# Optimization experiments

Measured on AMD Instinct MI355X. Metric: run time of the kernel, lower is better.

## Reference

```python
import jax, jax.numpy as jnp
import numpy as np
import math

QUERY_LEN = 64
VALUES_LEN = 64
NUM_HEADS = 16


def setup_inputs() -> dict:
    key = jax.random.key(0)
    k1, k2, k3, k4 = jax.random.split(key, 4)
    B, G, N = 2, 4, 1024
    D = QUERY_LEN * NUM_HEADS  # 1024
    queries = jax.random.normal(k1, (B, G, N, D), dtype=jnp.float32)
    keys = jax.random.normal(k2, (B, G, N, D), dtype=jnp.float32)
    values = jax.random.normal(k3, (B, G, N, VALUES_LEN * NUM_HEADS), dtype=jnp.float32)
    neuron_bank_connectivity_sub = jax.random.uniform(k4, (1, G, 1, N, N), dtype=jnp.float32)
    return {
        "queries": queries,
        "keys": keys,
        "values": values,
        "neuron_bank_connectivity_sub": neuron_bank_connectivity_sub,
    }


def reference(queries, keys, values, neuron_bank_connectivity_sub):
    B, G, N, _ = queries.shape
    H, dq, dv = NUM_HEADS, QUERY_LEN, VALUES_LEN
    # view last dim as (vec_len, num_heads), move heads forward: [B,G,H,N,d]
    q = queries.reshape(B, G, N, dq, H).transpose(0, 1, 4, 2, 3)
    k = keys.reshape(B, G, N, dq, H).transpose(0, 1, 4, 2, 3)
    v = values.reshape(B, G, N, dv, H).transpose(0, 1, 4, 2, 3)
    scores = jnp.einsum('bghnd,bghmd->bghnm', q, k) / math.sqrt(dq)
    probs = jax.nn.softmax(scores - neuron_bank_connectivity_sub, axis=-1)
    out = jnp.einsum('bghnm,bghmd->bghnd', probs, v)  # [B,G,H,N,dv]
    # Faithful to original: view() applied to the contiguous [B,G,H,N,dv] buffer
    return out.reshape(B, G, N, H * dv)
```

## Files before the change

kernel.cpp:

```cpp
#include <hip/hip_runtime.h>
#include <hip/hip_bf16.h>
#include <math.h>

#define B_ 2
#define G_ 4
#define N_ 1024
#define H_ 16
#define D_ 64
#define BG_ (B_*G_)
#define BGH_ (B_*G_*H_)
#define MK 64

typedef __bf16 bf16;
typedef bf16 bf16x8 __attribute__((ext_vector_type(8)));
typedef float f32x4 __attribute__((ext_vector_type(4)));

__global__ __launch_bounds__(256) void transpose_qk(const float* __restrict__ src,
                                                    bf16* __restrict__ dst) {
    int bx   = blockIdx.x;
    int bg   = bx >> 6;
    int tile = bx & 63;
    int t  = threadIdx.x;
    int h  = t & 15;
    int db = (t >> 4) & 7;
    int nh = t >> 7;
    const float* sb = src + (size_t)bg * N_ * 1024;
    bf16* ob = dst + ((size_t)(bg * H_ + h)) * N_ * D_;
#pragma unroll
    for (int np = 0; np < 8; ++np) {
        int n = tile * 16 + np * 2 + nh;
        const float* sr = sb + (size_t)n * 1024 + h;
        bf16x8 v;
#pragma unroll
        for (int k = 0; k < 8; ++k)
            v[k] = (bf16)sr[(db * 8 + k) * 16];
        *(bf16x8*)(ob + (size_t)n * D_ + db * 8) = v;
    }
}

__global__ __launch_bounds__(256) void transpose_v(const float* __restrict__ src,
                                                   bf16* __restrict__ dst) {
    int bx    = blockIdx.x;
    int dq    = bx & 3;
    int ntile = (bx >> 2) & 15;
    int bg    = bx >> 6;
    int t  = threadIdx.x;
    int h  = t & 15;
    int d  = dq * 16 + (t >> 4);
    const float* sb = src + (size_t)bg * N_ * 1024 + d * 16 + h;
    bf16* ob = dst + (((size_t)(bg * H_ + h)) * D_ + d) * N_;
#pragma unroll
    for (int n8 = 0; n8 < 8; ++n8) {
        int n = ntile * 64 + n8 * 8;
        bf16x8 v;
#pragma unroll
        for (int k = 0; k < 8; ++k)
            v[k] = (bf16)sb[(size_t)(n + k) * 1024];
        *(bf16x8*)(ob + n) = v;
    }
}

__global__ __launch_bounds__(256, 4) void flash_kernel(
    const bf16* __restrict__ qt, const bf16* __restrict__ kt, const bf16* __restrict__ vtT,
    const float* __restrict__ bias, float* __restrict__ out)
{
    __shared__ __attribute__((aligned(16))) bf16 k_lds[MK][72];
    __shared__ __attribute__((aligned(16))) bf16 v_lds[D_][72];
    __shared__ __attribute__((aligned(16))) bf16 p_lds[4][16][72];

    int tid  = threadIdx.x;
    int w    = tid >> 6;
    int lane = tid & 63;
    int quad = lane >> 4;
    int col  = lane & 15;

    int bgh = blockIdx.y;
    int n0  = blockIdx.x * 64;
    int g   = (bgh >> 4) & (G_ - 1);

    int qrow = n0 + w * 16 + col;
    const bf16* qbase = qt + ((size_t)bgh * N_ + qrow) * D_;
    bf16x8 aq0 = *(const bf16x8*)(qbase + quad * 8);
    bf16x8 aq1 = *(const bf16x8*)(qbase + 32 + quad * 8);

    f32x4 acc0 = {0,0,0,0}, acc1 = {0,0,0,0}, acc2 = {0,0,0,0}, acc3 = {0,0,0,0};
    float l_part[4] = {0, 0, 0, 0};

    int srow = tid >> 2;
    int soff = (tid & 3) * 16;
    const bf16* kp = kt + (size_t)bgh * N_ * D_ + (size_t)srow * D_ + soff;
    const bf16* vp = vtT + ((size_t)bgh * D_ + srow) * N_ + soff;
    const float* bias_base = bias + (size_t)g * N_ * N_;

    bf16x8 kr0 = *(const bf16x8*)(kp);
    bf16x8 kr1 = *(const bf16x8*)(kp + 8);
    bf16x8 vr0 = *(const bf16x8*)(vp);
    bf16x8 vr1 = *(const bf16x8*)(vp + 8);

    for (int m0 = 0; m0 < N_; m0 += MK) {
        __syncthreads();
        *(bf16x8*)(&k_lds[srow][soff])     = kr0;
        *(bf16x8*)(&k_lds[srow][soff + 8]) = kr1;
        *(bf16x8*)(&v_lds[srow][soff])     = vr0;
        *(bf16x8*)(&v_lds[srow][soff + 8]) = vr1;
        __syncthreads();

        if (m0 + MK < N_) {
            kp += MK * D_;  vp += MK;
            kr0 = *(const bf16x8*)(kp);
            kr1 = *(const bf16x8*)(kp + 8);
            vr0 = *(const bf16x8*)(vp);
            vr1 = *(const bf16x8*)(vp + 8);
        }

        float bl[4][4];
        const float* brow = bias_base + m0 + col;
#pragma unroll
        for (int r = 0; r < 4; ++r) {
            size_t ro = (size_t)(n0 + w * 16 + quad * 4 + r) * N_;
#pragma unroll
            for (int c = 0; c < 4; ++c)
                bl[r][c] = brow[ro + c * 16];
        }

        f32x4 s[4];
        f32x4 z = {0, 0, 0, 0};
#pragma unroll
        for (int c = 0; c < 4; ++c) {
            bf16x8 b0 = *(const bf16x8*)(&k_lds[c * 16 + col][quad * 8]);
            bf16x8 b1 = *(const bf16x8*)(&k_lds[c * 16 + col][32 + quad * 8]);
            s[c] = __builtin_amdgcn_mfma_f32_16x16x32_bf16(aq0, b0, z, 0, 0, 0);
            s[c] = __builtin_amdgcn_mfma_f32_16x16x32_bf16(aq1, b1, s[c], 0, 0, 0);
        }

#pragma unroll
        for (int c = 0; c < 4; ++c) {
#pragma unroll
            for (int r = 0; r < 4; ++r) {
                float p = __expf(s[c][r] * 0.125f - bl[r][c]);
                l_part[r] += p;
                p_lds[w][quad * 4 + r][c * 16 + col] = (bf16)p;
            }
        }

        bf16x8 ap0 = *(const bf16x8*)(&p_lds[w][col][quad * 8]);
        bf16x8 ap1 = *(const bf16x8*)(&p_lds[w][col][32 + quad * 8]);
        {
            bf16x8 bv00 = *(const bf16x8*)(&v_lds[col][quad * 8]);
            bf16x8 bv01 = *(const bf16x8*)(&v_lds[col][32 + quad * 8]);
            acc0 = __builtin_amdgcn_mfma_f32_16x16x32_bf16(ap0, bv00, acc0, 0, 0, 0);
            acc0 = __builtin_amdgcn_mfma_f32_16x16x32_bf16(ap1, bv01, acc0, 0, 0, 0);
            bf16x8 bv10 = *(const bf16x8*)(&v_lds[16 + col][quad * 8]);
            bf16x8 bv11 = *(const bf16x8*)(&v_lds[16 + col][32 + quad * 8]);
            acc1 = __builtin_amdgcn_mfma_f32_16x16x32_bf16(ap0, bv10, acc1, 0, 0, 0);
            acc1 = __builtin_amdgcn_mfma_f32_16x16x32_bf16(ap1, bv11, acc1, 0, 0, 0);
            bf16x8 bv20 = *(const bf16x8*)(&v_lds[32 + col][quad * 8]);
            bf16x8 bv21 = *(const bf16x8*)(&v_lds[32 + col][32 + quad * 8]);
            acc2 = __builtin_amdgcn_mfma_f32_16x16x32_bf16(ap0, bv20, acc2, 0, 0, 0);
            acc2 = __builtin_amdgcn_mfma_f32_16x16x32_bf16(ap1, bv21, acc2, 0, 0, 0);
            bf16x8 bv30 = *(const bf16x8*)(&v_lds[48 + col][quad * 8]);
            bf16x8 bv31 = *(const bf16x8*)(&v_lds[48 + col][32 + quad * 8]);
            acc3 = __builtin_amdgcn_mfma_f32_16x16x32_bf16(ap0, bv30, acc3, 0, 0, 0);
            acc3 = __builtin_amdgcn_mfma_f32_16x16x32_bf16(ap1, bv31, acc3, 0, 0, 0);
        }
    }

#pragma unroll
    for (int r = 0; r < 4; ++r) {
#pragma unroll
        for (int off = 1; off <= 8; off <<= 1)
            l_part[r] += __shfl_xor(l_part[r], off, 64);
    }
#pragma unroll
    for (int r = 0; r < 4; ++r) {
        float inv = 1.0f / l_part[r];
        int rown = n0 + w * 16 + quad * 4 + r;
        float* obase = out + ((size_t)bgh * N_ + rown) * D_ + col;
        obase[0]  = acc0[r] * inv;
        obase[16] = acc1[r] * inv;
        obase[32] = acc2[r] * inv;
        obase[48] = acc3[r] * inv;
    }
}

__global__ __launch_bounds__(256) void naive_kernel(
    const float* __restrict__ q, const float* __restrict__ k,
    const float* __restrict__ v, const float* __restrict__ bias,
    float* __restrict__ out)
{
    __shared__ float sc[N_];
    __shared__ float red[256];
    __shared__ float qrow[64];
    int n = blockIdx.x;
    int bgh = blockIdx.y;
    int bg = bgh >> 4, h = bgh & 15;
    int g = bg & (G_ - 1);
    int tid = threadIdx.x;
    const float* qr = q + ((size_t)(bg * N_ + n)) * 1024;
    if (tid < 64) qrow[tid] = qr[tid * 16 + h];
    __syncthreads();
    const float* bb = bias + (size_t)g * N_ * N_ + (size_t)n * N_;
    for (int m = tid; m < N_; m += 256) {
        const float* kr = k + ((size_t)(bg * N_ + m)) * 1024 + h;
        float dot = 0.f;
        for (int d = 0; d < 64; ++d) dot += qrow[d] * kr[d * 16];
        sc[m] = dot * 0.125f - bb[m];
    }
    __syncthreads();
    float mx = -INFINITY;
    for (int m = tid; m < N_; m += 256) mx = fmaxf(mx, sc[m]);
    red[tid] = mx; __syncthreads();
    for (int s = 128; s > 0; s >>= 1) {
        if (tid < s) red[tid] = fmaxf(red[tid], red[tid + s]);
        __syncthreads();
    }
    float M = red[0]; __syncthreads();
    float sum = 0.f;
    for (int m = tid; m < N_; m += 256) { float e = __expf(sc[m] - M); sc[m] = e; sum += e; }
    red[tid] = sum; __syncthreads();
    for (int s = 128; s > 0; s >>= 1) {
        if (tid < s) red[tid] += red[tid + s];
        __syncthreads();
    }
    float L = red[0]; __syncthreads();
    int d = tid & 63, quarter = tid >> 6;
    float acc = 0.f;
    const float* vb = v + (size_t)bg * N_ * 1024 + d * 16 + h;
    for (int m = quarter * 256; m < quarter * 256 + 256; ++m) acc += sc[m] * vb[(size_t)m * 1024];
    red[tid] = acc; __syncthreads();
    if (tid < 64) {
        float o = (red[tid] + red[tid + 64] + red[tid + 128] + red[tid + 192]) / L;
        out[((size_t)bgh * N_ + n) * 64 + d] = o;
    }
}

extern "C" void kernel_launch(void* const* d_in, const int* in_sizes, int n_in,
                              void* d_out, int out_size, void* d_ws, size_t ws_size,
                              hipStream_t stream) {
    const float* q    = (const float*)d_in[0];
    const float* k    = (const float*)d_in[1];
    const float* v    = (const float*)d_in[2];
    const float* bias = (const float*)d_in[3];
    float* out = (float*)d_out;

    const size_t elems = (size_t)BGH_ * N_ * D_;
    const size_t need  = 3 * elems * sizeof(bf16);

    if (ws_size >= need) {
        bf16* qt  = (bf16*)d_ws;
        bf16* ktb = qt + elems;
        bf16* vtT = ktb + elems;
        transpose_qk<<<BG_ * (N_ / 16), 256, 0, stream>>>(q, qt);
        transpose_qk<<<BG_ * (N_ / 16), 256, 0, stream>>>(k, ktb);
        transpose_v<<<BG_ * 16 * 4, 256, 0, stream>>>(v, vtT);
        dim3 grid(N_ / 64, BGH_);
        flash_kernel<<<grid, 256, 0, stream>>>(qt, ktb, vtT, bias, out);
    } else {
        dim3 grid(N_, BGH_);
        naive_kernel<<<grid, 256, 0, stream>>>(q, k, v, bias, out);
    }
}
```

Before: 234.6 us.

## Fuse QKV transposes via LDS staging and prefetch bias in flash loop

Replaces the three separate strided-gather transpose kernels with one fused kernel. It reads rows with coalesced float4 loads, stages them through LDS, and writes the head-major bf16 layouts, folding the softmax scale and log2e into Q. The flash kernel fully unrolls the key loop and double-buffers the bias loads one tile ahead in registers, and uses exp2 with an fma in place of expf. This targets uncoalesced transpose reads, extra launches and bias load latency, at the cost of more registers and an LDS-heavy transpose with possible bank conflicts on the V path.

```diff
diff --git a/kernel.cpp b/kernel.cpp
--- a/kernel.cpp
+++ b/kernel.cpp
@@ -10,53 +10,71 @@
 #define BG_ (B_*G_)
 #define BGH_ (B_*G_*H_)
 #define MK 64
+#define LOG2E 1.44269504f
+#define QSCALE (0.125f * LOG2E)
 
 typedef __bf16 bf16;
 typedef bf16 bf16x8 __attribute__((ext_vector_type(8)));
 typedef float f32x4 __attribute__((ext_vector_type(4)));
 
-__global__ __launch_bounds__(256) void transpose_qk(const float* __restrict__ src,
-                                                    bf16* __restrict__ dst) {
-    int bx   = blockIdx.x;
-    int bg   = bx >> 6;
-    int tile = bx & 63;
-    int t  = threadIdx.x;
-    int h  = t & 15;
-    int db = (t >> 4) & 7;
-    int nh = t >> 7;
-    const float* sb = src + (size_t)bg * N_ * 1024;
-    bf16* ob = dst + ((size_t)(bg * H_ + h)) * N_ * D_;
-#pragma unroll
-    for (int np = 0; np < 8; ++np) {
-        int n = tile * 16 + np * 2 + nh;
-        const float* sr = sb + (size_t)n * 1024 + h;
-        bf16x8 v;
-#pragma unroll
-        for (int k = 0; k < 8; ++k)
-            v[k] = (bf16)sr[(db * 8 + k) * 16];
-        *(bf16x8*)(ob + (size_t)n * D_ + db * 8) = v;
-    }
-}
-
-__global__ __launch_bounds__(256) void transpose_v(const float* __restrict__ src,
-                                                   bf16* __restrict__ dst) {
-    int bx    = blockIdx.x;
-    int dq    = bx & 3;
-    int ntile = (bx >> 2) & 15;
-    int bg    = bx >> 6;
-    int t  = threadIdx.x;
-    int h  = t & 15;
-    int d  = dq * 16 + (t >> 4);
-    const float* sb = src + (size_t)bg * N_ * 1024 + d * 16 + h;
-    bf16* ob = dst + (((size_t)(bg * H_ + h)) * D_ + d) * N_;
-#pragma unroll
-    for (int n8 = 0; n8 < 8; ++n8) {
-        int n = ntile * 64 + n8 * 8;
-        bf16x8 v;
-#pragma unroll
-        for (int k = 0; k < 8; ++k)
-            v[k] = (bf16)sb[(size_t)(n + k) * 1024];
-        *(bf16x8*)(ob + n) = v;
+#define HS 1160
+#define NS 72
+
+__global__ __launch_bounds__(256) void transpose_fused(
+    const float* __restrict__ q, const float* __restrict__ k, const float* __restrict__ v,
+    bf16* __restrict__ qt, bf16* __restrict__ ktb, bf16* __restrict__ vtT)
+{
+    __shared__ __attribute__((aligned(16))) bf16 lds[16 * HS];
+    int bx = blockIdx.x;
+    int tensor = bx >> 9;
+    int rr = bx & 511;
+    int bg = rr >> 6;
+    int tile = rr & 63;
+    int n0 = tile * 16;
+    int t = threadIdx.x;
+
+    const float* src = (tensor == 0) ? q : (tensor == 1) ? k : v;
+    float scale = (tensor == 0) ? QSCALE : 1.0f;
+    const float* sb = src + (size_t)bg * N_ * 1024 + (size_t)n0 * 1024;
+
+    int h0 = 4 * (t & 3);
+    int d  = t >> 2;
+    int wbase = h0 * HS + d;
+#pragma unroll 4
+    for (int i = 0; i < 16; ++i) {
+        float4 val = ((const float4*)(sb + (size_t)i * 1024))[t];
+        bf16* p = &lds[wbase + i * NS];
+        p[0]        = (bf16)(val.x * scale);
+        p[HS]       = (bf16)(val.y * scale);
+        p[2 * HS]   = (bf16)(val.z * scale);
+        p[3 * HS]   = (bf16)(val.w * scale);
+    }
+    __syncthreads();
+
+    if (tensor < 2) {
+        bf16* dst = (tensor == 0) ? qt : ktb;
+        int n  = (t >> 3) & 15;
+        int db = t & 7;
+        int hb = t >> 7;
+#pragma unroll
+        for (int i = 0; i < 8; ++i) {
+            int h = 2 * i + hb;
+            bf16x8 vv = *(const bf16x8*)(&lds[h * HS + n * NS + db * 8]);
+            *(bf16x8*)(dst + (((size_t)(bg * H_ + h)) * N_ + n0 + n) * D_ + db * 8) = vv;
+        }
+    } else {
+        int dd = t & 63;
+        int nc = (t >> 6) & 1;
+        int hb = t >> 7;
+#pragma unroll
+        for (int i = 0; i < 8; ++i) {
+            int h = 2 * i + hb;
+            bf16x8 vv;
+#pragma unroll
+            for (int jj = 0; jj < 8; ++jj)
+                vv[jj] = lds[h * HS + (nc * 8 + jj) * NS + dd];
+            *(bf16x8*)(vtT + (((size_t)(bg * H_ + h)) * D_ + dd) * N_ + n0 + nc * 8) = vv;
+        }
     }
 }
 
@@ -90,14 +108,31 @@
     int soff = (tid & 3) * 16;
     const bf16* kp = kt + (size_t)bgh * N_ * D_ + (size_t)srow * D_ + soff;
     const bf16* vp = vtT + ((size_t)bgh * D_ + srow) * N_ + soff;
-    const float* bias_base = bias + (size_t)g * N_ * N_;
+
+    const float* bptr[4];
+#pragma unroll
+    for (int r = 0; r < 4; ++r)
+        bptr[r] = bias + (size_t)g * N_ * N_
+                + (size_t)(n0 + w * 16 + quad * 4 + r) * N_ + col;
 
     bf16x8 kr0 = *(const bf16x8*)(kp);
     bf16x8 kr1 = *(const bf16x8*)(kp + 8);
     bf16x8 vr0 = *(const bf16x8*)(vp);
     bf16x8 vr1 = *(const bf16x8*)(vp + 8);
 
-    for (int m0 = 0; m0 < N_; m0 += MK) {
+    float blA[16], blB[16];
+#pragma unroll
+    for (int r = 0; r < 4; ++r)
+#pragma unroll
+        for (int c = 0; c < 4; ++c)
+            blA[r * 4 + c] = bptr[r][c * 16];
+
+#pragma unroll
+    for (int it = 0; it < 16; ++it) {
+        const int m0 = it * MK;
+        float (&cur)[16] = (it & 1) ? blB : blA;
+        float (&nxt)[16] = (it & 1) ? blA : blB;
+
         __syncthreads();
         *(bf16x8*)(&k_lds[srow][soff])     = kr0;
         *(bf16x8*)(&k_lds[srow][soff + 8]) = kr1;
@@ -105,22 +140,17 @@
         *(bf16x8*)(&v_lds[srow][soff + 8]) = vr1;
         __syncthreads();
 
-        if (m0 + MK < N_) {
+        if (it < 15) {
             kp += MK * D_;  vp += MK;
             kr0 = *(const bf16x8*)(kp);
             kr1 = *(const bf16x8*)(kp + 8);
             vr0 = *(const bf16x8*)(vp);
             vr1 = *(const bf16x8*)(vp + 8);
-        }
-
-        float bl[4][4];
-        const float* brow = bias_base + m0 + col;
-#pragma unroll
-        for (int r = 0; r < 4; ++r) {
-            size_t ro = (size_t)(n0 + w * 16 + quad * 4 + r) * N_;
-#pragma unroll
-            for (int c = 0; c < 4; ++c)
-                bl[r][c] = brow[ro + c * 16];
+#pragma unroll
+            for (int r = 0; r < 4; ++r)
+#pragma unroll
+                for (int c = 0; c < 4; ++c)
+                    nxt[r * 4 + c] = bptr[r][m0 + MK + c * 16];
         }
 
         f32x4 s[4];
@@ -137,7 +167,8 @@
         for (int c = 0; c < 4; ++c) {
 #pragma unroll
             for (int r = 0; r < 4; ++r) {
-                float p = __expf(s[c][r] * 0.125f - bl[r][c]);
+                float p = __builtin_amdgcn_exp2f(
+                    __builtin_fmaf(-LOG2E, cur[r * 4 + c], s[c][r]));
                 l_part[r] += p;
                 p_lds[w][quad * 4 + r][c * 16 + col] = (bf16)p;
             }
@@ -145,24 +176,22 @@
 
         bf16x8 ap0 = *(const bf16x8*)(&p_lds[w][col][quad * 8]);
         bf16x8 ap1 = *(const bf16x8*)(&p_lds[w][col][32 + quad * 8]);
-        {
-            bf16x8 bv00 = *(const bf16x8*)(&v_lds[col][quad * 8]);
-            bf16x8 bv01 = *(const bf16x8*)(&v_lds[col][32 + quad * 8]);
-            acc0 = __builtin_amdgcn_mfma_f32_16x16x32_bf16(ap0, bv00, acc0, 0, 0, 0);
-            acc0 = __builtin_amdgcn_mfma_f32_16x16x32_bf16(ap1, bv01, acc0, 0, 0, 0);
-            bf16x8 bv10 = *(const bf16x8*)(&v_lds[16 + col][quad * 8]);
-            bf16x8 bv11 = *(const bf16x8*)(&v_lds[16 + col][32 + quad * 8]);
-            acc1 = __builtin_amdgcn_mfma_f32_16x16x32_bf16(ap0, bv10, acc1, 0, 0, 0);
-            acc1 = __builtin_amdgcn_mfma_f32_16x16x32_bf16(ap1, bv11, acc1, 0, 0, 0);
-            bf16x8 bv20 = *(const bf16x8*)(&v_lds[32 + col][quad * 8]);
-            bf16x8 bv21 = *(const bf16x8*)(&v_lds[32 + col][32 + quad * 8]);
-            acc2 = __builtin_amdgcn_mfma_f32_16x16x32_bf16(ap0, bv20, acc2, 0, 0, 0);
-            acc2 = __builtin_amdgcn_mfma_f32_16x16x32_bf16(ap1, bv21, acc2, 0, 0, 0);
-            bf16x8 bv30 = *(const bf16x8*)(&v_lds[48 + col][quad * 8]);
-            bf16x8 bv31 = *(const bf16x8*)(&v_lds[48 + col][32 + quad * 8]);
-            acc3 = __builtin_amdgcn_mfma_f32_16x16x32_bf16(ap0, bv30, acc3, 0, 0, 0);
-            acc3 = __builtin_amdgcn_mfma_f32_16x16x32_bf16(ap1, bv31, acc3, 0, 0, 0);
-        }
+        bf16x8 bv00 = *(const bf16x8*)(&v_lds[col][quad * 8]);
+        bf16x8 bv01 = *(const bf16x8*)(&v_lds[col][32 + quad * 8]);
+        acc0 = __builtin_amdgcn_mfma_f32_16x16x32_bf16(ap0, bv00, acc0, 0, 0, 0);
+        acc0 = __builtin_amdgcn_mfma_f32_16x16x32_bf16(ap1, bv01, acc0, 0, 0, 0);
+        bf16x8 bv10 = *(const bf16x8*)(&v_lds[16 + col][quad * 8]);
+        bf16x8 bv11 = *(const bf16x8*)(&v_lds[16 + col][32 + quad * 8]);
+        acc1 = __builtin_amdgcn_mfma_f32_16x16x32_bf16(ap0, bv10, acc1, 0, 0, 0);
+        acc1 = __builtin_amdgcn_mfma_f32_16x16x32_bf16(ap1, bv11, acc1, 0, 0, 0);
+        bf16x8 bv20 = *(const bf16x8*)(&v_lds[32 + col][quad * 8]);
+        bf16x8 bv21 = *(const bf16x8*)(&v_lds[32 + col][32 + quad * 8]);
+        acc2 = __builtin_amdgcn_mfma_f32_16x16x32_bf16(ap0, bv20, acc2, 0, 0, 0);
+        acc2 = __builtin_amdgcn_mfma_f32_16x16x32_bf16(ap1, bv21, acc2, 0, 0, 0);
+        bf16x8 bv30 = *(const bf16x8*)(&v_lds[48 + col][quad * 8]);
+        bf16x8 bv31 = *(const bf16x8*)(&v_lds[48 + col][32 + quad * 8]);
+        acc3 = __builtin_amdgcn_mfma_f32_16x16x32_bf16(ap0, bv30, acc3, 0, 0, 0);
+        acc3 = __builtin_amdgcn_mfma_f32_16x16x32_bf16(ap1, bv31, acc3, 0, 0, 0);
     }
 
 #pragma unroll
@@ -250,9 +279,7 @@
         bf16* qt  = (bf16*)d_ws;
         bf16* ktb = qt + elems;
         bf16* vtT = ktb + elems;
-        transpose_qk<<<BG_ * (N_ / 16), 256, 0, stream>>>(q, qt);
-        transpose_qk<<<BG_ * (N_ / 16), 256, 0, stream>>>(k, ktb);
-        transpose_v<<<BG_ * 16 * 4, 256, 0, stream>>>(v, vtT);
+        transpose_fused<<<3 * 512, 256, 0, stream>>>(q, k, v, qt, ktb, vtT);
         dim3 grid(N_ / 64, BGH_);
         flash_kernel<<<grid, 256, 0, stream>>>(qt, ktb, vtT, bias, out);
     } else {
```

After: 477.9 us. 104% more time.
